# Optimization experiments

Hardware: AMD Instinct MI355X
Metric: run time of the kernel (lower is better)

The kernel has to match this reference:

```python
import jax, jax.numpy as jnp
import numpy as np

TOKENS, IN_F, OUT_F = 8192, 4096, 4096
ZERO_POINT = 0      # input zero point (int8)
OUT_ZP = 0          # output zero point (int8)
OUT_SCALE = 0.05    # output quant scale


def setup_inputs() -> dict:
    key = jax.random.key(0)
    k1, k2, k3, k4 = jax.random.split(key, 4)
    x = jax.random.randint(k1, (TOKENS, IN_F), -128, 128, dtype=jnp.int32).astype(jnp.int8)
    # weight stored as [in_features, out_features] (module.weight.t() quantized in from_float)
    weight = jax.random.randint(k2, (IN_F, OUT_F), -127, 128, dtype=jnp.int32).astype(jnp.int8)
    bias = jax.random.randint(k3, (1, OUT_F), -1000, 1000, dtype=jnp.int32)
    gemm_scales = jax.random.uniform(k4, (1, OUT_F), minval=1e-4, maxval=2e-4, dtype=jnp.float32)
    return {"x": x, "weight": weight, "bias": bias, "gemm_scales": gemm_scales}


def reference(x, weight, bias, gemm_scales):
    # int8 -> int32 -> fp32, subtract input zero point
    a = (x.astype(jnp.int32) - ZERO_POINT).astype(jnp.float32)   # [T, IN]
    w = weight.astype(jnp.float32)                               # [IN, OUT]
    gemm_o = (a @ w + bias.astype(jnp.float32)) * gemm_scales / OUT_SCALE  # [T, OUT]
    out = jnp.clip(gemm_o + OUT_ZP, -128, 127).astype(jnp.int8)
    return out
```

## Files before the change

### kernel.cpp

```cpp
#include <hip/hip_runtime.h>
#include <stdint.h>

#define TOKENS 8192
#define IN_F   4096
#define OUT_F  4096

#define BM 256
#define BN 256
#define BK 64
#define NK (IN_F / BK)
#define THREADS 512

typedef int v4i __attribute__((ext_vector_type(4)));

#define GLOBAL_AS __attribute__((address_space(1)))
#define LDS_AS    __attribute__((address_space(3)))

__global__ __launch_bounds__(256) void pack_x_kernel(const int* __restrict__ x32,
                                                     uint8_t* __restrict__ x8) {
  int t = blockIdx.x * 256 + threadIdx.x;
  const int4 v = ((const int4*)x32)[t];
  uint32_t p = (uint32_t)(v.x & 0xFF)
             | ((uint32_t)(v.y & 0xFF) << 8)
             | ((uint32_t)(v.z & 0xFF) << 16)
             | ((uint32_t)(v.w & 0xFF) << 24);
  ((uint32_t*)x8)[t] = p;
}

__global__ __launch_bounds__(256) void packT_w_kernel(const int* __restrict__ w32,
                                                      uint8_t* __restrict__ wt8) {
  int tn = (blockIdx.x & 63) * 64;
  int tk = (blockIdx.x >> 6) * 64;
  int t = threadIdx.x;
  int n  = tn + (t >> 2);
  int k0 = tk + (t & 3) * 16;
  uint32_t words[4];
#pragma unroll
  for (int w = 0; w < 4; ++w) {
    uint32_t acc = 0;
#pragma unroll
    for (int j = 0; j < 4; ++j) {
      int val = w32[(size_t)(k0 + w * 4 + j) * OUT_F + n];
      acc |= (uint32_t)(val & 0xFF) << (8 * j);
    }
    words[w] = acc;
  }
  uint4 o = make_uint4(words[0], words[1], words[2], words[3]);
  *(uint4*)(wt8 + (size_t)n * IN_F + k0) = o;
}

__global__ __launch_bounds__(THREADS, 2) void gemm_i8_kernel(const uint8_t* __restrict__ A,
                                                             const uint8_t* __restrict__ BT,
                                                             const int* __restrict__ bias,
                                                             const float* __restrict__ scales,
                                                             int* __restrict__ out) {
  __shared__ __align__(16) uint8_t lds[4 * 32768];

  const int t    = threadIdx.x;
  const int lane = t & 63;
  const int w    = t >> 6;
  const int wr   = w >> 2;
  const int wc   = w & 3;
  const int fr   = lane & 15;
  const int fq   = lane >> 4;

  int bid = blockIdx.x;
  int swz = (bid & 7) * 64 + (bid >> 3);
  int bm = swz >> 4;
  int bn = swz & 15;

  const int lsz  = t ^ ((t >> 3) & 7);
  const int srow = lsz >> 2;
  const int scol = (lsz & 3) * 16;
  const size_t gA0 = (size_t)(bm * BM + srow) * IN_F + scol;
  const size_t gA1 = gA0 + (size_t)128 * IN_F;
  const size_t gB0 = (size_t)(bn * BN + srow) * IN_F + scol;
  const size_t gB1 = gB0 + (size_t)128 * IN_F;
  const int ldst = t * 16;

  auto stageA = [&](int j) {
    uint8_t* sb = lds + (j & 3) * 32768;
    const int k0 = j * BK;
    __builtin_amdgcn_global_load_lds((const GLOBAL_AS void*)(A + gA0 + k0),
                                     (LDS_AS void*)(sb + ldst),          16, 0, 0);
    __builtin_amdgcn_global_load_lds((const GLOBAL_AS void*)(A + gA1 + k0),
                                     (LDS_AS void*)(sb + 8192 + ldst),   16, 0, 0);
  };
  auto stageB = [&](int j) {
    uint8_t* sb = lds + (j & 3) * 32768;
    const int k0 = j * BK;
    __builtin_amdgcn_global_load_lds((const GLOBAL_AS void*)(BT + gB0 + k0),
                                     (LDS_AS void*)(sb + 16384 + ldst),  16, 0, 0);
    __builtin_amdgcn_global_load_lds((const GLOBAL_AS void*)(BT + gB1 + k0),
                                     (LDS_AS void*)(sb + 24576 + ldst),  16, 0, 0);
  };

  int aoff[8], boff[4];
#pragma unroll
  for (int m = 0; m < 8; ++m) {
    int row = wr * 128 + m * 16 + fr;
    int half = row >> 7, rl = row & 127;
    int b = rl * 64 + fq * 16;
    b ^= ((rl >> 1) & 7) << 4;
    aoff[m] = half * 8192 + b;
  }
#pragma unroll
  for (int n = 0; n < 4; ++n) {
    int row = wc * 64 + n * 16 + fr;
    int half = row >> 7, rl = row & 127;
    int b = rl * 64 + fq * 16;
    b ^= ((rl >> 1) & 7) << 4;
    boff[n] = 16384 + half * 8192 + b;
  }

  v4i acc[8][4];
  const v4i vzero = {0, 0, 0, 0};
#pragma unroll
  for (int m = 0; m < 8; ++m)
#pragma unroll
    for (int n = 0; n < 4; ++n) acc[m][n] = vzero;

  stageA(0); stageB(0); stageA(1); stageB(1); stageA(2); stageB(2);

#define SLICE(i, VM, DOSTAGE)                                                   \
  asm volatile("s_waitcnt vmcnt(" #VM ")" ::: "memory");                        \
  asm volatile("s_barrier" ::: "memory");                                       \
  {                                                                             \
    const uint8_t* sb = lds + ((i) & 3) * 32768;                                \
    v4i bf[4], af[4], af2[4];                                                   \
    _Pragma("unroll") for (int n = 0; n < 4; ++n)                               \
      bf[n] = *(const v4i*)(sb + boff[n]);                                      \
    _Pragma("unroll") for (int m = 0; m < 4; ++m)                               \
      af[m] = *(const v4i*)(sb + aoff[m]);                                      \
    if (DOSTAGE) stageA((i) + 3);                                               \
    asm volatile("s_barrier" ::: "memory");                                     \
    asm volatile("s_waitcnt lgkmcnt(0)" ::: "memory");                          \
    __builtin_amdgcn_sched_barrier(0);                                          \
    __builtin_amdgcn_s_setprio(1);                                              \
    _Pragma("unroll") for (int m = 0; m < 4; ++m)                               \
      _Pragma("unroll") for (int n = 0; n < 4; ++n)                             \
        acc[m][n] = __builtin_amdgcn_mfma_i32_16x16x64_i8(af[m], bf[n],         \
                                                          acc[m][n], 0, 0, 0); \
    __builtin_amdgcn_s_setprio(0);                                              \
    asm volatile("s_barrier" ::: "memory");                                     \
    _Pragma("unroll") for (int m = 0; m < 4; ++m)                               \
      af2[m] = *(const v4i*)(sb + aoff[4 + m]);                                 \
    if (DOSTAGE) stageB((i) + 3);                                               \
    asm volatile("s_barrier" ::: "memory");                                     \
    asm volatile("s_waitcnt lgkmcnt(0)" ::: "memory");                          \
    __builtin_amdgcn_sched_barrier(0);                                          \
    __builtin_amdgcn_s_setprio(1);                                              \
    _Pragma("unroll") for (int m = 0; m < 4; ++m)                               \
      _Pragma("unroll") for (int n = 0; n < 4; ++n)                             \
        acc[4 + m][n] = __builtin_amdgcn_mfma_i32_16x16x64_i8(af2[m], bf[n],    \
                                                      acc[4 + m][n], 0, 0, 0); \
    __builtin_amdgcn_s_setprio(0);                                              \
  }

  for (int i = 0; i < NK - 3; ++i) {
    SLICE(i, 8, true)
  }
  SLICE(NK - 3, 8, false)
  SLICE(NK - 2, 4, false)
  SLICE(NK - 1, 0, false)
#undef SLICE

#pragma unroll
  for (int n = 0; n < 4; ++n) {
    const int gn  = bn * BN + wc * 64 + n * 16 + fr;
    const int bsv = bias[gn];
    const float sc = scales[gn] * 20.0f;
#pragma unroll
    for (int m = 0; m < 8; ++m) {
      const int gm0 = bm * BM + wr * 128 + m * 16 + fq * 4;
#pragma unroll
      for (int r = 0; r < 4; ++r) {
        float g = (float)(acc[m][n][r] + bsv) * sc;
        g = fminf(fmaxf(g, -128.0f), 127.0f);
        out[(size_t)(gm0 + r) * OUT_F + gn] = (int)g;
      }
    }
  }
}

extern "C" void kernel_launch(void* const* d_in, const int* in_sizes, int n_in,
                              void* d_out, int out_size, void* d_ws, size_t ws_size,
                              hipStream_t stream) {
  const int*   x32    = (const int*)d_in[0];
  const int*   w32    = (const int*)d_in[1];
  const int*   bias   = (const int*)d_in[2];
  const float* scales = (const float*)d_in[3];
  int* out = (int*)d_out;

  uint8_t* x8  = (uint8_t*)d_ws;
  uint8_t* wt8 = (uint8_t*)d_ws + (size_t)TOKENS * IN_F;

  pack_x_kernel<<<(TOKENS * IN_F / 4) / 256, 256, 0, stream>>>(x32, x8);
  packT_w_kernel<<<(OUT_F / 64) * (IN_F / 64), 256, 0, stream>>>(w32, wt8);
  gemm_i8_kernel<<<(TOKENS / BM) * (OUT_F / BN), THREADS, 0, stream>>>(x8, wt8, bias, scales, out);
}
```

Before: 196.1 us.

## Double-buffer MFMA fragments in registers and cut per-slice barriers to one

Restructures the K loop so each slice loads the A and B fragments for the next slice into a second register set while the current slice's MFMAs run. It also merges the A and B global-to-LDS staging into one call per slice. This drops three of the four s_barriers and the explicit lgkmcnt(0) waits per K step, so LDS reads and global loads can overlap with compute instead of serialising around barriers. The cost is more live VGPRs for the extra fragment set, which could spill or reduce occupancy under the 2-blocks launch bound. The single barrier per slice now also has to protect the 4-deep LDS ring from being overwritten while it is still being read.

```diff
diff --git a/kernel.cpp b/kernel.cpp
--- a/kernel.cpp
+++ b/kernel.cpp
@@ -78,17 +78,13 @@
   const size_t gB1 = gB0 + (size_t)128 * IN_F;
   const int ldst = t * 16;
 
-  auto stageA = [&](int j) {
+  auto stage = [&](int j) {
     uint8_t* sb = lds + (j & 3) * 32768;
     const int k0 = j * BK;
     __builtin_amdgcn_global_load_lds((const GLOBAL_AS void*)(A + gA0 + k0),
                                      (LDS_AS void*)(sb + ldst),          16, 0, 0);
     __builtin_amdgcn_global_load_lds((const GLOBAL_AS void*)(A + gA1 + k0),
                                      (LDS_AS void*)(sb + 8192 + ldst),   16, 0, 0);
-  };
-  auto stageB = [&](int j) {
-    uint8_t* sb = lds + (j & 3) * 32768;
-    const int k0 = j * BK;
     __builtin_amdgcn_global_load_lds((const GLOBAL_AS void*)(BT + gB0 + k0),
                                      (LDS_AS void*)(sb + 16384 + ldst),  16, 0, 0);
     __builtin_amdgcn_global_load_lds((const GLOBAL_AS void*)(BT + gB1 + k0),
@@ -120,50 +116,55 @@
 #pragma unroll
     for (int n = 0; n < 4; ++n) acc[m][n] = vzero;
 
-  stageA(0); stageB(0); stageA(1); stageB(1); stageA(2); stageB(2);
-
-#define SLICE(i, VM, DOSTAGE)                                                   \
-  asm volatile("s_waitcnt vmcnt(" #VM ")" ::: "memory");                        \
-  asm volatile("s_barrier" ::: "memory");                                       \
+#define BODY(i, VM, DOSTAGE, DONEXT, afCUR, bfCUR, afNXT, bfNXT)                \
   {                                                                             \
-    const uint8_t* sb = lds + ((i) & 3) * 32768;                                \
-    v4i bf[4], af[4], af2[4];                                                   \
-    _Pragma("unroll") for (int n = 0; n < 4; ++n)                               \
-      bf[n] = *(const v4i*)(sb + boff[n]);                                      \
+    asm volatile("s_waitcnt vmcnt(" #VM ")" ::: "memory");                      \
+    asm volatile("s_barrier" ::: "memory");                                     \
+    const uint8_t* sb  = lds + ((i) & 3) * 32768;                               \
+    const uint8_t* sbn = lds + (((i) + 1) & 3) * 32768;                         \
+    v4i af2[4];                                                                 \
     _Pragma("unroll") for (int m = 0; m < 4; ++m)                               \
-      af[m] = *(const v4i*)(sb + aoff[m]);                                      \
-    if (DOSTAGE) stageA((i) + 3);                                               \
-    asm volatile("s_barrier" ::: "memory");                                     \
-    asm volatile("s_waitcnt lgkmcnt(0)" ::: "memory");                          \
+      af2[m] = *(const v4i*)(sb + aoff[4 + m]);                                 \
+    if (DONEXT) {                                                               \
+      _Pragma("unroll") for (int n = 0; n < 4; ++n)                             \
+        bfNXT[n] = *(const v4i*)(sbn + boff[n]);                                \
+      _Pragma("unroll") for (int m = 0; m < 4; ++m)                             \
+        afNXT[m] = *(const v4i*)(sbn + aoff[m]);                                \
+    }                                                                           \
+    if (DOSTAGE) stage((i) + 3);                                                \
     __builtin_amdgcn_sched_barrier(0);                                          \
     __builtin_amdgcn_s_setprio(1);                                              \
     _Pragma("unroll") for (int m = 0; m < 4; ++m)                               \
       _Pragma("unroll") for (int n = 0; n < 4; ++n)                             \
-        acc[m][n] = __builtin_amdgcn_mfma_i32_16x16x64_i8(af[m], bf[n],         \
-                                                          acc[m][n], 0, 0, 0); \
+        acc[m][n] = __builtin_amdgcn_mfma_i32_16x16x64_i8(afCUR[m], bfCUR[n],   \
+                                                          acc[m][n], 0, 0, 0);  \
     __builtin_amdgcn_s_setprio(0);                                              \
-    asm volatile("s_barrier" ::: "memory");                                     \
-    _Pragma("unroll") for (int m = 0; m < 4; ++m)                               \
-      af2[m] = *(const v4i*)(sb + aoff[4 + m]);                                 \
-    if (DOSTAGE) stageB((i) + 3);                                               \
-    asm volatile("s_barrier" ::: "memory");                                     \
-    asm volatile("s_waitcnt lgkmcnt(0)" ::: "memory");                          \
-    __builtin_amdgcn_sched_barrier(0);                                          \
     __builtin_amdgcn_s_setprio(1);                                              \
     _Pragma("unroll") for (int m = 0; m < 4; ++m)                               \
       _Pragma("unroll") for (int n = 0; n < 4; ++n)                             \
-        acc[4 + m][n] = __builtin_amdgcn_mfma_i32_16x16x64_i8(af2[m], bf[n],    \
-                                                      acc[4 + m][n], 0, 0, 0); \
+        acc[4 + m][n] = __builtin_amdgcn_mfma_i32_16x16x64_i8(af2[m], bfCUR[n], \
+                                                      acc[4 + m][n], 0, 0, 0);  \
     __builtin_amdgcn_s_setprio(0);                                              \
   }
 
-  for (int i = 0; i < NK - 3; ++i) {
-    SLICE(i, 8, true)
-  }
-  SLICE(NK - 3, 8, false)
-  SLICE(NK - 2, 4, false)
-  SLICE(NK - 1, 0, false)
-#undef SLICE
+  stage(0); stage(1); stage(2);
+  asm volatile("s_waitcnt vmcnt(8)" ::: "memory");
+  asm volatile("s_barrier" ::: "memory");
+  v4i afC[4], bfC[4], afN[4], bfN[4];
+#pragma unroll
+  for (int n = 0; n < 4; ++n) bfC[n] = *(const v4i*)(lds + boff[n]);
+#pragma unroll
+  for (int m = 0; m < 4; ++m) afC[m] = *(const v4i*)(lds + aoff[m]);
+
+  for (int i = 0; i < 60; i += 2) {
+    BODY(i,     4, true,  true,  afC, bfC, afN, bfN)
+    BODY(i + 1, 4, true,  true,  afN, bfN, afC, bfC)
+  }
+  BODY(60, 4, true,  true,  afC, bfC, afN, bfN)
+  BODY(61, 4, false, true,  afN, bfN, afC, bfC)
+  BODY(62, 0, false, true,  afC, bfC, afN, bfN)
+  BODY(63, 0, false, false, afN, bfN, afC, bfC)
+#undef BODY
 
 #pragma unroll
   for (int n = 0; n < 4; ++n) {
```

After: 189.7 us. -3.3%, faster.
